# Optimization experiments

Measured on AMD Instinct MI355X. Metric: run time of the kernel, lower is better.

The kernel has to match this reference:

```python
import jax, jax.numpy as jnp
import numpy as np

BLOCK = 128  # block_size=(128,128) from MoeFP8Matmul
E, H, I = 8, 2048, 2816  # experts, hidden, intermediate
T, K = 512, 2  # tokens, top-k

_FP8 = getattr(jnp, "float8_e4m3fn", jnp.float32)

def _dequant(w, s):
    # w: [N, Kd] fp8 values (stored fp32), s: [N//128, Kd//128] inverse scales
    s_full = jnp.repeat(jnp.repeat(s, BLOCK, axis=-2), BLOCK, axis=-1)
    return w * s_full

def setup_inputs() -> dict:
    key = jax.random.key(0)
    ks = jax.random.split(key, 7)
    x = jax.random.normal(ks[0], (T, H), dtype=jnp.float32)
    topk_ids = jax.random.randint(ks[1], (T, K), 0, E, dtype=jnp.int64)
    topk_weights = jax.random.uniform(ks[2], (T, K), dtype=jnp.float32)
    # fp8-representable weight values (round-trip through e4m3)
    w13 = (jax.random.normal(ks[3], (E, 2 * I, H), dtype=jnp.float32) * 0.5)
    w13_fp8 = w13.astype(_FP8).astype(jnp.float32)
    w2 = (jax.random.normal(ks[4], (E, H, I), dtype=jnp.float32) * 0.5)
    w2_fp8 = w2.astype(_FP8).astype(jnp.float32)
    w13_scale = jax.random.uniform(ks[5], (E, (2 * I) // BLOCK, H // BLOCK),
                                   dtype=jnp.float32, minval=0.5, maxval=1.5)
    w2_scale = jax.random.uniform(ks[6], (E, H // BLOCK, I // BLOCK),
                                  dtype=jnp.float32, minval=0.5, maxval=1.5)
    return {"x": x, "topk_ids": topk_ids, "topk_weights": topk_weights,
            "w13_fp8": w13_fp8, "w13_scale": w13_scale,
            "w2_fp8": w2_fp8, "w2_scale": w2_scale}

def reference(x, topk_ids, topk_weights, w13_fp8, w13_scale, w2_fp8, w2_scale):
    # Per-expert block-FP8 dequant then grouped SwiGLU MoE GEMM, weighted-summed by router.
    out = jnp.zeros_like(x)
    for e in range(E):  # small fixed expert count
        W13 = _dequant(w13_fp8[e], w13_scale[e])   # [2I, H]
        W2 = _dequant(w2_fp8[e], w2_scale[e])      # [H, I]
        h = x @ W13.T                              # [T, 2I]
        gate, up = jnp.split(h, 2, axis=-1)
        act = jax.nn.silu(gate) * up               # [T, I]
        oe = act @ W2.T                            # [T, H]
        coef = jnp.sum(jnp.where(topk_ids == e, topk_weights, 0.0), axis=-1)  # [T]
        out = out + coef[:, None] * oe
    return out
```

## Files before the change

kernel.cpp:

```cpp
#include <hip/hip_runtime.h>
#include <hip/hip_bf16.h>
#include <cstdint>
#include <cstddef>

#define E_   8
#define H_   2048
#define I_   2816
#define T_   512
#define NPAIR 1024

#define TM   192
#define TN   32
#define BK   64
#define MT_  3

typedef __attribute__((ext_vector_type(8))) short          bf16x8;
typedef __attribute__((ext_vector_type(4))) float          f32x4;
typedef __attribute__((ext_vector_type(8))) unsigned short u16x8;

__device__ __forceinline__ unsigned short f2bf(float f){
  union { float f; unsigned u; } a; a.f = f;
  unsigned u = a.u;
  unsigned r = u + 0x7fffu + ((u >> 16) & 1u);
  return (unsigned short)(r >> 16);
}

__device__ __forceinline__ void cvt4(u16x8& dst, int base, const float4 v, float s){
  __hip_bfloat162 p0 = __float22bfloat162_rn(float2{v.x*s, v.y*s});
  __hip_bfloat162 p1 = __float22bfloat162_rn(float2{v.z*s, v.w*s});
  union { __hip_bfloat162 b; unsigned u; } a0{p0}, a1{p1};
  dst[base+0] = (unsigned short)(a0.u & 0xffff);
  dst[base+1] = (unsigned short)(a0.u >> 16);
  dst[base+2] = (unsigned short)(a1.u & 0xffff);
  dst[base+3] = (unsigned short)(a1.u >> 16);
}

__device__ __forceinline__ bf16x8 u2b(u16x8 v){
  union { u16x8 u; bf16x8 b; } x; x.u = v; return x.b;
}

__device__ __forceinline__ void gload_lds16(const void* g, void* l){
  __builtin_amdgcn_global_load_lds(
      (const __attribute__((address_space(1))) unsigned int*)g,
      (__attribute__((address_space(3))) unsigned int*)l, 16, 0, 0);
}

__global__ void route_kernel(const int* __restrict__ ids,
                             int* __restrict__ offs, int* __restrict__ ptok,
                             int* __restrict__ sop){
  __shared__ int scnt[E_];
  __shared__ int scur[E_];
  const int tid = threadIdx.x;
  if (tid < E_) scnt[tid] = 0;
  __syncthreads();
  const int e = ids[tid];
  atomicAdd(&scnt[e], 1);
  __syncthreads();
  if (tid == 0){
    int s = 0;
    for (int i = 0; i < E_; i++){ offs[i] = s; scur[i] = s; s += scnt[i]; }
    offs[E_] = s;
  }
  __syncthreads();
  const int pos = atomicAdd(&scur[e], 1);
  ptok[pos] = tid >> 1;
  sop[tid]  = pos;
}

__global__ void prep_kernel(const float* __restrict__ x, const int* __restrict__ ptok,
                            unsigned short* __restrict__ xg){
  const int slot = blockIdx.x;
  const int tok  = ptok[slot];
  const int k0   = threadIdx.x * 8;
  const float4 v0 = *(const float4*)(x + (size_t)tok*H_ + k0);
  const float4 v1 = *(const float4*)(x + (size_t)tok*H_ + k0 + 4);
  u16x8 o;
  cvt4(o, 0, v0, 1.f);
  cvt4(o, 4, v1, 1.f);
  *(u16x8*)(xg + (size_t)slot*H_ + k0) = o;
}

__global__ __launch_bounds__(256, 3)
void gemm1_kernel(const unsigned short* __restrict__ xg, const float* __restrict__ w13,
                  const float* __restrict__ s13, const int* __restrict__ offs,
                  unsigned short* __restrict__ act)
{
  const int e   = blockIdx.x;
  const int off = offs[e];
  const int cnt = offs[e+1] - off;
  const int m0  = blockIdx.z * TM;
  if (m0 >= cnt) return;
  const int rows = min(TM, cnt - m0);
  const int nb   = blockIdx.y * TN;

  __shared__ __align__(16) float Bs[3][2*TN][BK];

  const int tid  = threadIdx.x;
  const int wv   = tid >> 6;
  const int lane = tid & 63;
  const int quad = lane >> 4;
  const int l16  = lane & 15;

  const float* w13e = w13 + (size_t)e * (2*I_) * H_;
  const float* s13e = s13 + (size_t)e * (2*I_/128) * (H_/128);

  const int s0row = (nb >> 7) * (H_/128);
  const int s1row = ((I_/128) + (nb >> 7)) * (H_/128);

  const char* srcP[4];
  #pragma unroll
  for (int j = 0; j < 4; j++){
    const int rl = wv*16 + j*4 + (lane >> 4);
    const int gr = (rl < TN) ? (nb + rl) : (I_ + nb + (rl - TN));
    const int cb = ((lane & 15) << 4) ^ ((rl & 7) << 4);
    srcP[j] = (const char*)(w13e + (size_t)gr * H_) + cb;
  }
  auto stage = [&](int t, int slot){
    #pragma unroll
    for (int j = 0; j < 4; j++)
      gload_lds16(srcP[j] + (size_t)t * (BK*4), &Bs[slot][wv*16 + j*4][0]);
  };

  const unsigned short* aP[MT_];
  #pragma unroll
  for (int mt = 0; mt < MT_; mt++){
    int sl = off + m0 + wv*(TM/4) + mt*16 + l16;
    sl = min(sl, NPAIR - 1);
    aP[mt] = xg + (size_t)sl * H_ + quad*8;
  }

  f32x4 acc[2][MT_][2];
  #pragma unroll
  for (int h = 0; h < 2; h++)
    #pragma unroll
    for (int mt = 0; mt < MT_; mt++)
      #pragma unroll
      for (int nt = 0; nt < 2; nt++)
        acc[h][mt][nt] = (f32x4){0.f, 0.f, 0.f, 0.f};

  bf16x8 A0[2][MT_], A1[2][MT_];
  auto loadA = [&](int t, bf16x8 (*A)[MT_]){
    #pragma unroll
    for (int kk = 0; kk < 2; kk++)
      #pragma unroll
      for (int mt = 0; mt < MT_; mt++)
        A[kk][mt] = *(const bf16x8*)(aP[mt] + t*BK + kk*32);
  };

  auto comp = [&](int slot, bf16x8 (*A)[MT_], float sg, float su){
    #pragma unroll
    for (int kk = 0; kk < 2; kk++)
      #pragma unroll
      for (int hh = 0; hh < 2; hh++){
        const float s = hh ? su : sg;
        #pragma unroll
        for (int nt = 0; nt < 2; nt++){
          const int row = hh*TN + nt*16 + l16;
          const int xr  = (row & 7) << 2;
          const int cb  = kk*32 + quad*8;
          const float4 F0 = *(const float4*)&Bs[slot][row][cb ^ xr];
          const float4 F1 = *(const float4*)&Bs[slot][row][(cb + 4) ^ xr];
          u16x8 o; cvt4(o, 0, F0, s); cvt4(o, 4, F1, s);
          const bf16x8 bv = u2b(o);
          #pragma unroll
          for (int mt = 0; mt < MT_; mt++)
            acc[hh][mt][nt] = __builtin_amdgcn_mfma_f32_16x16x32_bf16(A[kk][mt], bv, acc[hh][mt][nt], 0, 0, 0);
        }
      }
  };

  const int NITER = H_/BK;
  loadA(0, A0);
  stage(0, 0);
  stage(1, 1);
  asm volatile("s_waitcnt vmcnt(4)" ::: "memory");
  __builtin_amdgcn_s_barrier();
  stage(2, 2);
  loadA(1, A1);
  comp(0, A0, s13e[s0row], s13e[s1row]);

  int cs = 1, ss = 0;
  for (int t = 1; t < NITER-1; t++){
    asm volatile("s_waitcnt vmcnt(10)" ::: "memory");
    __builtin_amdgcn_s_barrier();
    if (t+2 < NITER) stage(t+2, ss);
    loadA(t+1, (t & 1) ? A0 : A1);
    const float sg = s13e[s0row + (t >> 1)];
    const float su = s13e[s1row + (t >> 1)];
    comp(cs, (t & 1) ? A1 : A0, sg, su);
    cs = (cs == 2) ? 0 : cs + 1;
    ss = (ss == 2) ? 0 : ss + 1;
  }
  {
    asm volatile("s_waitcnt vmcnt(6)" ::: "memory");
    __builtin_amdgcn_s_barrier();
    const int t = NITER-1;
    comp(cs, (t & 1) ? A1 : A0, s13e[s0row + (t >> 1)], s13e[s1row + (t >> 1)]);
  }

  #pragma unroll
  for (int mt = 0; mt < MT_; mt++){
    #pragma unroll
    for (int nt = 0; nt < 2; nt++){
      #pragma unroll
      for (int r = 0; r < 4; r++){
        const int m = wv*(TM/4) + mt*16 + quad*4 + r;
        if (m < rows){
          const float g = acc[0][mt][nt][r];
          const float u = acc[1][mt][nt][r];
          const float sg2 = g / (1.f + __expf(-g));
          act[(size_t)(off + m0 + m)*I_ + (nb + nt*16 + l16)] = f2bf(sg2 * u);
        }
      }
    }
  }
}

__global__ __launch_bounds__(256, 3)
void gemm2_kernel(const unsigned short* __restrict__ act, const float* __restrict__ w2,
                  const float* __restrict__ s2, const int* __restrict__ offs,
                  float* __restrict__ buf)
{
  const int e   = blockIdx.x;
  const int off = offs[e];
  const int cnt = offs[e+1] - off;
  const int m0  = blockIdx.z * TM;
  if (m0 >= cnt) return;
  const int rows = min(TM, cnt - m0);
  const int nb   = blockIdx.y * TN;

  __shared__ __align__(16) float Bs[3][TN][BK];

  const int tid  = threadIdx.x;
  const int wv   = tid >> 6;
  const int lane = tid & 63;
  const int quad = lane >> 4;
  const int l16  = lane & 15;

  const float* w2e = w2 + (size_t)e * H_ * I_;
  const float* s2e = s2 + (size_t)e * (H_/128) * (I_/128);
  const int srow  = (nb >> 7) * (I_/128);

  const char* srcP[2];
  #pragma unroll
  for (int j = 0; j < 2; j++){
    const int rl = wv*8 + j*4 + (lane >> 4);
    const int cb = ((lane & 15) << 4) ^ ((rl & 7) << 4);
    srcP[j] = (const char*)(w2e + (size_t)(nb + rl) * I_) + cb;
  }
  auto stage = [&](int t, int slot){
    #pragma unroll
    for (int j = 0; j < 2; j++)
      gload_lds16(srcP[j] + (size_t)t * (BK*4), &Bs[slot][wv*8 + j*4][0]);
  };

  const unsigned short* aP[MT_];
  #pragma unroll
  for (int mt = 0; mt < MT_; mt++){
    int sl = off + m0 + wv*(TM/4) + mt*16 + l16;
    sl = min(sl, NPAIR - 1);
    aP[mt] = act + (size_t)sl * I_ + quad*8;
  }

  f32x4 acc[MT_][2];
  #pragma unroll
  for (int mt = 0; mt < MT_; mt++)
    #pragma unroll
    for (int nt = 0; nt < 2; nt++)
      acc[mt][nt] = (f32x4){0.f, 0.f, 0.f, 0.f};

  bf16x8 A0[2][MT_], A1[2][MT_];
  auto loadA = [&](int t, bf16x8 (*A)[MT_]){
    #pragma unroll
    for (int kk = 0; kk < 2; kk++)
      #pragma unroll
      for (int mt = 0; mt < MT_; mt++)
        A[kk][mt] = *(const bf16x8*)(aP[mt] + t*BK + kk*32);
  };

  auto comp = [&](int slot, bf16x8 (*A)[MT_], float s){
    #pragma unroll
    for (int kk = 0; kk < 2; kk++)
      #pragma unroll
      for (int nt = 0; nt < 2; nt++){
        const int row = nt*16 + l16;
        const int xr  = (row & 7) << 2;
        const int cb  = kk*32 + quad*8;
        const float4 F0 = *(const float4*)&Bs[slot][row][cb ^ xr];
        const float4 F1 = *(const float4*)&Bs[slot][row][(cb + 4) ^ xr];
        u16x8 o; cvt4(o, 0, F0, s); cvt4(o, 4, F1, s);
        const bf16x8 bv = u2b(o);
        #pragma unroll
        for (int mt = 0; mt < MT_; mt++)
          acc[mt][nt] = __builtin_amdgcn_mfma_f32_16x16x32_bf16(A[kk][mt], bv, acc[mt][nt], 0, 0, 0);
      }
  };

  const int NITER = I_/BK;
  loadA(0, A0);
  stage(0, 0);
  stage(1, 1);
  asm volatile("s_waitcnt vmcnt(2)" ::: "memory");
  __builtin_amdgcn_s_barrier();
  stage(2, 2);
  loadA(1, A1);
  comp(0, A0, s2e[srow]);

  int cs = 1, ss = 0;
  for (int t = 1; t < NITER-1; t++){
    asm volatile("s_waitcnt vmcnt(8)" ::: "memory");
    __builtin_amdgcn_s_barrier();
    if (t+2 < NITER) stage(t+2, ss);
    loadA(t+1, (t & 1) ? A0 : A1);
    comp(cs, (t & 1) ? A1 : A0, s2e[srow + (t >> 1)]);
    cs = (cs == 2) ? 0 : cs + 1;
    ss = (ss == 2) ? 0 : ss + 1;
  }
  {
    asm volatile("s_waitcnt vmcnt(6)" ::: "memory");
    __builtin_amdgcn_s_barrier();
    const int t = NITER-1;
    comp(cs, (t & 1) ? A1 : A0, s2e[srow + (t >> 1)]);
  }

  #pragma unroll
  for (int mt = 0; mt < MT_; mt++){
    #pragma unroll
    for (int nt = 0; nt < 2; nt++){
      #pragma unroll
      for (int r = 0; r < 4; r++){
        const int m = wv*(TM/4) + mt*16 + quad*4 + r;
        if (m < rows)
          buf[(size_t)(off + m0 + m)*H_ + (nb + nt*16 + l16)] = acc[mt][nt][r];
      }
    }
  }
}

__global__ void combine_kernel(const float* __restrict__ buf, const int* __restrict__ sop,
                               const float* __restrict__ tw, float* __restrict__ out){
  const int gid = blockIdx.x*256 + threadIdx.x;
  const int t = gid >> 9;
  const int c = gid & 511;
  const int s0 = sop[2*t], s1 = sop[2*t+1];
  const float w0 = tw[2*t], w1 = tw[2*t+1];
  const float4 v0 = ((const float4*)buf)[(size_t)s0*(H_/4) + c];
  const float4 v1 = ((const float4*)buf)[(size_t)s1*(H_/4) + c];
  float4 o;
  o.x = w0*v0.x + w1*v1.x;
  o.y = w0*v0.y + w1*v1.y;
  o.z = w0*v0.z + w1*v1.z;
  o.w = w0*v0.w + w1*v1.w;
  ((float4*)out)[gid] = o;
}

extern "C" void kernel_launch(void* const* d_in, const int* in_sizes, int n_in,
                              void* d_out, int out_size, void* d_ws, size_t ws_size,
                              hipStream_t stream){
  const float* x   = (const float*)d_in[0];
  const int*   ids = (const int*)  d_in[1];
  const float* tw  = (const float*)d_in[2];
  const float* w13 = (const float*)d_in[3];
  const float* s13 = (const float*)d_in[4];
  const float* w2  = (const float*)d_in[5];
  const float* s2  = (const float*)d_in[6];
  float* out = (float*)d_out;

  char* ws = (char*)d_ws;
  int* offs = (int*)ws;
  int* ptok = (int*)(ws + 64);
  int* sop  = (int*)(ws + 64 + 4096);
  unsigned short* xg  = (unsigned short*)(ws + 16384);
  float*          buf = (float*)(ws + 16384);
  unsigned short* act = (unsigned short*)(ws + 16384 + (size_t)NPAIR*H_*4);

  route_kernel  <<<1, NPAIR, 0, stream>>>(ids, offs, ptok, sop);
  prep_kernel   <<<NPAIR, 256, 0, stream>>>(x, ptok, xg);
  gemm1_kernel  <<<dim3(E_, I_/TN, (NPAIR + TM - 1)/TM), 256, 0, stream>>>(xg, w13, s13, offs, act);
  gemm2_kernel  <<<dim3(E_, H_/TN, (NPAIR + TM - 1)/TM), 256, 0, stream>>>(act, w2, s2, offs, buf);
  combine_kernel<<<(T_*H_/4)/256, 256, 0, stream>>>(buf, sop, tw, out);
}
```

Baseline: 700.9 us.

## Deepen GEMM pipelines to four LDS stages with inline-asm A-operand prefetch

Both MoE GEMM kernels move from a 3-slot to a 4-slot LDS ring for the fp32 weight tiles. A operands now come through raw global_load_dwordx4 inline asm into four rotating register buffers, prefetched two iterations ahead. The main loop is unrolled by four with explicit vmcnt waits and sched_barrier, so that memory latency is hidden better behind MFMA work. The cost is more LDS and registers per block, and occupancy is lowered from 3 to 2 blocks per SIMD. The hand-counted vmcnt values and tail steps are fragile if the number of outstanding loads changes.

New measurement: 702.1 us. About the same (+0.2%).

```diff
diff --git a/kernel.cpp b/kernel.cpp
--- a/kernel.cpp
+++ b/kernel.cpp
@@ -16,6 +16,7 @@
 
 typedef __attribute__((ext_vector_type(8))) short          bf16x8;
 typedef __attribute__((ext_vector_type(4))) float          f32x4;
+typedef __attribute__((ext_vector_type(4))) int            i32x4;
 typedef __attribute__((ext_vector_type(8))) unsigned short u16x8;
 
 __device__ __forceinline__ unsigned short f2bf(float f){
@@ -44,6 +45,17 @@
       (const __attribute__((address_space(1))) unsigned int*)g,
       (__attribute__((address_space(3))) unsigned int*)l, 16, 0, 0);
 }
+
+__device__ __forceinline__ i32x4 gload16(const void* p){
+  i32x4 r;
+  asm volatile("global_load_dwordx4 %0, %1, off" : "=v"(r) : "v"(p));
+  return r;
+}
+
+#define WAIT_BAR(N)                                            \
+  asm volatile("s_waitcnt vmcnt(" #N ")" ::: "memory");        \
+  __builtin_amdgcn_sched_barrier(0);                           \
+  __builtin_amdgcn_s_barrier();
 
 __global__ void route_kernel(const int* __restrict__ ids,
                              int* __restrict__ offs, int* __restrict__ ptok,
@@ -80,7 +92,7 @@
   *(u16x8*)(xg + (size_t)slot*H_ + k0) = o;
 }
 
-__global__ __launch_bounds__(256, 3)
+__global__ __launch_bounds__(256, 2)
 void gemm1_kernel(const unsigned short* __restrict__ xg, const float* __restrict__ w13,
                   const float* __restrict__ s13, const int* __restrict__ offs,
                   unsigned short* __restrict__ act)
@@ -93,7 +105,7 @@
   const int rows = min(TM, cnt - m0);
   const int nb   = blockIdx.y * TN;
 
-  __shared__ __align__(16) float Bs[3][2*TN][BK];
+  __shared__ __align__(16) float Bs[4][2*TN][BK];
 
   const int tid  = threadIdx.x;
   const int wv   = tid >> 6;
@@ -138,16 +150,16 @@
       for (int nt = 0; nt < 2; nt++)
         acc[h][mt][nt] = (f32x4){0.f, 0.f, 0.f, 0.f};
 
-  bf16x8 A0[2][MT_], A1[2][MT_];
-  auto loadA = [&](int t, bf16x8 (*A)[MT_]){
+  i32x4 A0[6], A1[6], A2[6], A3[6];
+  auto loadA = [&](int t, i32x4* A){
     #pragma unroll
     for (int kk = 0; kk < 2; kk++)
       #pragma unroll
       for (int mt = 0; mt < MT_; mt++)
-        A[kk][mt] = *(const bf16x8*)(aP[mt] + t*BK + kk*32);
-  };
-
-  auto comp = [&](int slot, bf16x8 (*A)[MT_], float sg, float su){
+        A[kk*MT_ + mt] = gload16(aP[mt] + t*BK + kk*32);
+  };
+
+  auto comp = [&](int slot, const i32x4* A, float sg, float su){
     #pragma unroll
     for (int kk = 0; kk < 2; kk++)
       #pragma unroll
@@ -163,8 +175,10 @@
           u16x8 o; cvt4(o, 0, F0, s); cvt4(o, 4, F1, s);
           const bf16x8 bv = u2b(o);
           #pragma unroll
-          for (int mt = 0; mt < MT_; mt++)
-            acc[hh][mt][nt] = __builtin_amdgcn_mfma_f32_16x16x32_bf16(A[kk][mt], bv, acc[hh][mt][nt], 0, 0, 0);
+          for (int mt = 0; mt < MT_; mt++){
+            const bf16x8 av = *(const bf16x8*)&A[kk*MT_ + mt];
+            acc[hh][mt][nt] = __builtin_amdgcn_mfma_f32_16x16x32_bf16(av, bv, acc[hh][mt][nt], 0, 0, 0);
+          }
         }
       }
   };
@@ -173,30 +187,33 @@
   loadA(0, A0);
   stage(0, 0);
   stage(1, 1);
-  asm volatile("s_waitcnt vmcnt(4)" ::: "memory");
-  __builtin_amdgcn_s_barrier();
+  loadA(1, A1);
   stage(2, 2);
-  loadA(1, A1);
+  WAIT_BAR(14)
+  loadA(2, A2);
+  stage(3, 3);
   comp(0, A0, s13e[s0row], s13e[s1row]);
 
-  int cs = 1, ss = 0;
-  for (int t = 1; t < NITER-1; t++){
-    asm volatile("s_waitcnt vmcnt(10)" ::: "memory");
-    __builtin_amdgcn_s_barrier();
-    if (t+2 < NITER) stage(t+2, ss);
-    loadA(t+1, (t & 1) ? A0 : A1);
-    const float sg = s13e[s0row + (t >> 1)];
-    const float su = s13e[s1row + (t >> 1)];
-    comp(cs, (t & 1) ? A1 : A0, sg, su);
-    cs = (cs == 2) ? 0 : cs + 1;
-    ss = (ss == 2) ? 0 : ss + 1;
-  }
-  {
-    asm volatile("s_waitcnt vmcnt(6)" ::: "memory");
-    __builtin_amdgcn_s_barrier();
-    const int t = NITER-1;
-    comp(cs, (t & 1) ? A1 : A0, s13e[s0row + (t >> 1)], s13e[s1row + (t >> 1)]);
-  }
+#define G1_STEP(T, AL, AC)                                        \
+  { WAIT_BAR(14)                                                  \
+    loadA((T)+2, AL);                                             \
+    stage((T)+3, ((T)+3) & 3);                                    \
+    comp((T) & 3, AC, s13e[s0row + ((T) >> 1)], s13e[s1row + ((T) >> 1)]); }
+
+  for (int tb = 1; tb <= 25; tb += 4){
+    G1_STEP(tb+0, A3, A1)
+    G1_STEP(tb+1, A0, A2)
+    G1_STEP(tb+2, A1, A3)
+    G1_STEP(tb+3, A2, A0)
+  }
+  { WAIT_BAR(14)
+    loadA(31, A3);
+    comp(1, A1, s13e[s0row + 14], s13e[s1row + 14]); }
+  { WAIT_BAR(10)
+    comp(2, A2, s13e[s0row + 15], s13e[s1row + 15]); }
+  { WAIT_BAR(0)
+    comp(3, A3, s13e[s0row + 15], s13e[s1row + 15]); }
+#undef G1_STEP
 
   #pragma unroll
   for (int mt = 0; mt < MT_; mt++){
@@ -216,7 +233,7 @@
   }
 }
 
-__global__ __launch_bounds__(256, 3)
+__global__ __launch_bounds__(256, 2)
 void gemm2_kernel(const unsigned short* __restrict__ act, const float* __restrict__ w2,
                   const float* __restrict__ s2, const int* __restrict__ offs,
                   float* __restrict__ buf)
@@ -229,7 +246,7 @@
   const int rows = min(TM, cnt - m0);
   const int nb   = blockIdx.y * TN;
 
-  __shared__ __align__(16) float Bs[3][TN][BK];
+  __shared__ __align__(16) float Bs[4][TN][BK];
 
   const int tid  = threadIdx.x;
   const int wv   = tid >> 6;
@@ -269,16 +286,16 @@
     for (int nt = 0; nt < 2; nt++)
       acc[mt][nt] = (f32x4){0.f, 0.f, 0.f, 0.f};
 
-  bf16x8 A0[2][MT_], A1[2][MT_];
-  auto loadA = [&](int t, bf16x8 (*A)[MT_]){
+  i32x4 A0[6], A1[6], A2[6], A3[6];
+  auto loadA = [&](int t, i32x4* A){
     #pragma unroll
     for (int kk = 0; kk < 2; kk++)
       #pragma unroll
       for (int mt = 0; mt < MT_; mt++)
-        A[kk][mt] = *(const bf16x8*)(aP[mt] + t*BK + kk*32);
-  };
-
-  auto comp = [&](int slot, bf16x8 (*A)[MT_], float s){
+        A[kk*MT_ + mt] = gload16(aP[mt] + t*BK + kk*32);
+  };
+
+  auto comp = [&](int slot, const i32x4* A, float s){
     #pragma unroll
     for (int kk = 0; kk < 2; kk++)
       #pragma unroll
@@ -291,8 +308,10 @@
         u16x8 o; cvt4(o, 0, F0, s); cvt4(o, 4, F1, s);
         const bf16x8 bv = u2b(o);
         #pragma unroll
-        for (int mt = 0; mt < MT_; mt++)
-          acc[mt][nt] = __builtin_amdgcn_mfma_f32_16x16x32_bf16(A[kk][mt], bv, acc[mt][nt], 0, 0, 0);
+        for (int mt = 0; mt < MT_; mt++){
+          const bf16x8 av = *(const bf16x8*)&A[kk*MT_ + mt];
+          acc[mt][nt] = __builtin_amdgcn_mfma_f32_16x16x32_bf16(av, bv, acc[mt][nt], 0, 0, 0);
+        }
       }
   };
 
@@ -300,28 +319,33 @@
   loadA(0, A0);
   stage(0, 0);
   stage(1, 1);
-  asm volatile("s_waitcnt vmcnt(2)" ::: "memory");
-  __builtin_amdgcn_s_barrier();
+  loadA(1, A1);
   stage(2, 2);
-  loadA(1, A1);
+  WAIT_BAR(10)
+  loadA(2, A2);
+  stage(3, 3);
   comp(0, A0, s2e[srow]);
 
-  int cs = 1, ss = 0;
-  for (int t = 1; t < NITER-1; t++){
-    asm volatile("s_waitcnt vmcnt(8)" ::: "memory");
-    __builtin_amdgcn_s_barrier();
-    if (t+2 < NITER) stage(t+2, ss);
-    loadA(t+1, (t & 1) ? A0 : A1);
-    comp(cs, (t & 1) ? A1 : A0, s2e[srow + (t >> 1)]);
-    cs = (cs == 2) ? 0 : cs + 1;
-    ss = (ss == 2) ? 0 : ss + 1;
-  }
-  {
-    asm volatile("s_waitcnt vmcnt(6)" ::: "memory");
-    __builtin_amdgcn_s_barrier();
-    const int t = NITER-1;
-    comp(cs, (t & 1) ? A1 : A0, s2e[srow + (t >> 1)]);
-  }
+#define G2_STEP(T, AL, AC)                                        \
+  { WAIT_BAR(10)                                                  \
+    loadA((T)+2, AL);                                             \
+    stage((T)+3, ((T)+3) & 3);                                    \
+    comp((T) & 3, AC, s2e[srow + ((T) >> 1)]); }
+
+  for (int tb = 1; tb <= 37; tb += 4){
+    G2_STEP(tb+0, A3, A1)
+    G2_STEP(tb+1, A0, A2)
+    G2_STEP(tb+2, A1, A3)
+    G2_STEP(tb+3, A2, A0)
+  }
+  { WAIT_BAR(10)
+    loadA(43, A3);
+    comp(1, A1, s2e[srow + 20]); }
+  { WAIT_BAR(8)
+    comp(2, A2, s2e[srow + 21]); }
+  { WAIT_BAR(0)
+    comp(3, A3, s2e[srow + 21]); }
+#undef G2_STEP
 
   #pragma unroll
   for (int mt = 0; mt < MT_; mt++){
```
